# Optimization experiments

Measured on AMD Instinct MI355X. Metric: run time of the kernel, lower is better.

The kernel has to match this reference:

```python
import jax, jax.numpy as jnp
import numpy as np

S, B, H, E, V, T = 160, 64, 1024, 512, 64, 16


def setup_inputs() -> dict:
    key = jax.random.key(0)
    ks = jax.random.split(key, 13)
    g = lambda k, shape, scale: jax.random.normal(k, shape, jnp.float32) * scale
    return dict(
        encoder_h0=g(ks[0], (1, B, H), 1.0),
        encoder_c0=g(ks[1], (1, B, H), 1.0),
        encoder_outputs=g(ks[2], (S, B, H), 1.0),
        encoder_lens=jax.random.randint(ks[3], (B,), 1, S + 1),
        tok_embed=g(ks[4], (1, E), 0.02),
        embed=g(ks[5], (V, E), 0.02),
        W_ih=g(ks[6], (4 * H, E), 1.0 / np.sqrt(E)),
        W_hh=g(ks[7], (4 * H, H), 1.0 / np.sqrt(H)),
        b_ih=jnp.zeros((4 * H,), jnp.float32),
        b_hh=jnp.zeros((4 * H,), jnp.float32),
        out_W=g(ks[8], (V, 2 * H), 1.0 / np.sqrt(2 * H)),
        out_b=jnp.zeros((V,), jnp.float32),
        enc_W=g(ks[9], (H, H), 1.0 / np.sqrt(H)),
        enc_b=jnp.zeros((H,), jnp.float32),
        dec_W=g(ks[10], (H, H), 1.0 / np.sqrt(H)),
        dec_b=jnp.zeros((H,), jnp.float32),
        attn_W=g(ks[11], (1, H), 1.0 / np.sqrt(H)),
        attn_b=jnp.zeros((1,), jnp.float32),
    )


def reference(encoder_h0, encoder_c0, encoder_outputs, encoder_lens,
              tok_embed, embed, W_ih, W_hh, b_ih, b_hh,
              out_W, out_b, enc_W, enc_b, dec_W, dec_b, attn_W, attn_b):
    S_, B_, H_ = encoder_outputs.shape
    h0, c0 = encoder_h0[0], encoder_c0[0]          # [B,H]; source re-feeds encoder_hidden each step
    invalid = jnp.arange(S_)[None, :] >= encoder_lens[:, None]   # [B,S] True where masked
    NEG = jnp.float32(-1e9)

    def step(embed_tok, _):
        # LSTM cell, torch gate order (i, f, g, o)
        gates = embed_tok @ W_ih.T + b_ih + h0 @ W_hh.T + b_hh   # [B,4H]
        i, f, g, o = jnp.split(gates, 4, axis=-1)
        c = jax.nn.sigmoid(f) * c0 + jax.nn.sigmoid(i) * jnp.tanh(g)
        out = jax.nn.sigmoid(o) * jnp.tanh(c)                    # [B,H]
        # additive (Bahdanau) attention scores
        enc_t = jnp.einsum('sbh,kh->sbk', encoder_outputs, enc_W) + enc_b   # [S,B,H]
        dec_t = out @ dec_W.T + dec_b                                       # [B,H]
        scores = (jnp.tanh(enc_t + dec_t[None]) @ attn_W[0] + attn_b[0]).T # [B,S]
        attn = jax.nn.softmax(jnp.where(invalid, NEG, scores), axis=-1)    # [B,S]
        context = jnp.einsum('bs,sbh->bh', attn, encoder_outputs)          # [B,H]
        combined = jnp.concatenate([context, out], axis=-1)                # [B,2H]
        probs = jax.nn.softmax(combined @ out_W.T + out_b, axis=-1)
        probs = probs / jnp.sum(probs, axis=-1, keepdims=True)             # source renormalizes
        tok = jnp.argmax(probs, axis=-1)                                   # greedy decode
        onehot = jax.nn.one_hot(tok, probs.shape[-1], dtype=probs.dtype)
        neg_ent = jnp.sum(jax.lax.stop_gradient(probs) * jnp.log(probs + 1e-6), axis=-1)
        logp = jnp.log(jnp.sum(probs * onehot, axis=-1) + 1e-6)
        return embed[tok], (tok, attn, neg_ent, logp)

    start = jnp.broadcast_to(tok_embed[0], (B_, tok_embed.shape[1]))  # <SOS> embedding
    _, (toks, attns, negents, logps) = jax.lax.scan(step, start, None, length=T)
    predicted_tokens = toks                            # [T,B]
    context_total = jnp.transpose(attns, (1, 0, 2))    # [B,T,S] (attention maps, as in source)
    return predicted_tokens, context_total, jnp.sum(negents, axis=0), jnp.sum(logps, axis=0)
```

## Files before the change

### kernel.cpp

```cpp
#include <hip/hip_runtime.h>

#define S_ 160
#define B_ 64
#define H_ 1024
#define E_ 512
#define V_ 64
#define T_ 16
#define H4_ 4096

__device__ __forceinline__ float sigm(float x) { return 1.f / (1.f + expf(-x)); }

__global__ __launch_bounds__(256) void gemm_bt_128(
    const float* __restrict__ A, const float* __restrict__ Bm,
    const float* __restrict__ bias, float* __restrict__ Cd,
    int M, int N, int K)
{
    __shared__ float As[16][132];
    __shared__ float Bs[16][132];
    const int bn = blockIdx.x, bm = blockIdx.y;
    const int tid = threadIdx.x;
    const int lr = tid >> 1, lk = (tid & 1) * 8;
    const int tx4 = (tid & 15) * 4, ty4 = (tid >> 4) * 4;
    const float* Ap = A + (size_t)(bm * 128 + lr) * K + lk;
    const float* Bp = Bm + (size_t)(bn * 128 + lr) * K + lk;
    float acc[8][8] = {};
    for (int k0 = 0; k0 < K; k0 += 16) {
        float4 a0 = *(const float4*)(Ap + k0);
        float4 a1 = *(const float4*)(Ap + k0 + 4);
        float4 b0 = *(const float4*)(Bp + k0);
        float4 b1 = *(const float4*)(Bp + k0 + 4);
        __syncthreads();
        As[lk + 0][lr] = a0.x; As[lk + 1][lr] = a0.y; As[lk + 2][lr] = a0.z; As[lk + 3][lr] = a0.w;
        As[lk + 4][lr] = a1.x; As[lk + 5][lr] = a1.y; As[lk + 6][lr] = a1.z; As[lk + 7][lr] = a1.w;
        Bs[lk + 0][lr] = b0.x; Bs[lk + 1][lr] = b0.y; Bs[lk + 2][lr] = b0.z; Bs[lk + 3][lr] = b0.w;
        Bs[lk + 4][lr] = b1.x; Bs[lk + 5][lr] = b1.y; Bs[lk + 6][lr] = b1.z; Bs[lk + 7][lr] = b1.w;
        __syncthreads();
#pragma unroll
        for (int kk = 0; kk < 16; ++kk) {
            float a[8], b[8];
            *(float4*)(a)     = *(const float4*)&As[kk][ty4];
            *(float4*)(a + 4) = *(const float4*)&As[kk][64 + ty4];
            *(float4*)(b)     = *(const float4*)&Bs[kk][tx4];
            *(float4*)(b + 4) = *(const float4*)&Bs[kk][64 + tx4];
#pragma unroll
            for (int i = 0; i < 8; ++i)
#pragma unroll
                for (int j = 0; j < 8; ++j) acc[i][j] = fmaf(a[i], b[j], acc[i][j]);
        }
    }
#pragma unroll
    for (int i = 0; i < 8; ++i) {
        int row = bm * 128 + ((i < 4) ? (ty4 + i) : (64 + ty4 + i - 4));
#pragma unroll
        for (int j = 0; j < 8; ++j) {
            int col = bn * 128 + ((j < 4) ? (tx4 + j) : (64 + tx4 + j - 4));
            Cd[(size_t)row * N + col] = acc[i][j] + bias[col];
        }
    }
}

__device__ __forceinline__ void tile64(const float* __restrict__ Arow,
                                       const float* __restrict__ Brow,
                                       int K, float acc[4][4],
                                       float* __restrict__ As,
                                       float* __restrict__ Bs)
{
    const int tid = threadIdx.x;
    const int lr = tid >> 2, lc = (tid & 3) << 2;
    const int tx = tid & 15, ty = tid >> 4;
    for (int k0 = 0; k0 < K; k0 += 16) {
        float4 av = *(const float4*)(Arow + k0);
        float4 bv = *(const float4*)(Brow + k0);
        __syncthreads();
        As[lr * 17 + lc + 0] = av.x; As[lr * 17 + lc + 1] = av.y;
        As[lr * 17 + lc + 2] = av.z; As[lr * 17 + lc + 3] = av.w;
        Bs[lr * 17 + lc + 0] = bv.x; Bs[lr * 17 + lc + 1] = bv.y;
        Bs[lr * 17 + lc + 2] = bv.z; Bs[lr * 17 + lc + 3] = bv.w;
        __syncthreads();
#pragma unroll
        for (int kk = 0; kk < 16; ++kk) {
            float a[4], b[4];
#pragma unroll
            for (int i = 0; i < 4; ++i) a[i] = As[(ty * 4 + i) * 17 + kk];
#pragma unroll
            for (int j = 0; j < 4; ++j) b[j] = Bs[(tx * 4 + j) * 17 + kk];
#pragma unroll
            for (int i = 0; i < 4; ++i)
#pragma unroll
                for (int j = 0; j < 4; ++j) acc[i][j] = fmaf(a[i], b[j], acc[i][j]);
        }
    }
    __syncthreads();
}

__global__ __launch_bounds__(256) void gemm_part(
    const float* __restrict__ A, const float* __restrict__ Bm,
    float* __restrict__ Cpart, int M, int N, int K)
{
    __shared__ float smem[2176];
    const int bn = blockIdx.x, bm = blockIdx.y, kz = blockIdx.z, KS = gridDim.z;
    const int tid = threadIdx.x;
    const int lr = tid >> 2, lc = (tid & 3) << 2;
    const int tx = tid & 15, ty = tid >> 4;
    const int kLen = K / KS, k0base = kz * kLen;
    float acc[4][4] = {};
    tile64(A + (size_t)(bm * 64 + lr) * K + k0base + lc,
           Bm + (size_t)(bn * 64 + lr) * K + k0base + lc,
           kLen, acc, smem, smem + 1088);
    float* Cp = Cpart + (size_t)kz * M * N;
#pragma unroll
    for (int i = 0; i < 4; ++i) {
        int row = bm * 64 + ty * 4 + i;
#pragma unroll
        for (int j = 0; j < 4; ++j)
            Cp[(size_t)row * N + bn * 64 + tx * 4 + j] = acc[i][j];
    }
}

__global__ void reduce_partials(const float* __restrict__ Cpart, int KS,
                                const float* __restrict__ bias,
                                const float* __restrict__ bias2,
                                float* __restrict__ C, int MN, int N)
{
    int idx = blockIdx.x * 256 + threadIdx.x;
    if (idx >= MN) return;
    float v = 0.f;
    for (int z = 0; z < KS; ++z) v += Cpart[(size_t)z * MN + idx];
    int col = idx % N;
    if (bias)  v += bias[col];
    if (bias2) v += bias2[col];
    C[idx] = v;
}

__global__ void init_k(const float* __restrict__ embed, const float* __restrict__ tok_emb,
                       float* __restrict__ emb_ext,
                       float* __restrict__ negent, float* __restrict__ logp)
{
    int i = blockIdx.x * 256 + threadIdx.x;
    if (i < 128 * E_) {
        int r = i >> 9, c = i & (E_ - 1);
        emb_ext[i] = (r < 64) ? embed[r * E_ + c] : ((r == 64) ? tok_emb[c] : 0.f);
    }
    if (i < B_) { negent[i] = 0.f; logp[i] = 0.f; }
}

__global__ __launch_bounds__(256) void lstm_gather_k(
    const float* __restrict__ all_gates, const float* __restrict__ gates_sel,
    const float* __restrict__ hh_gates, const float* __restrict__ enc_c0,
    float* __restrict__ out_h, int t)
{
    int idx = blockIdx.x * 256 + threadIdx.x;
    int b = idx >> 10, h = idx & (H_ - 1);
    const float* ag = (t == 0) ? (all_gates + (size_t)64 * H4_)
                               : (gates_sel + (size_t)b * H4_);
    const float* hg = hh_gates + (size_t)b * H4_;
    float gi = ag[h]           + hg[h];
    float gf = ag[H_ + h]      + hg[H_ + h];
    float gg = ag[2 * H_ + h]  + hg[2 * H_ + h];
    float go = ag[3 * H_ + h]  + hg[3 * H_ + h];
    float cc = sigm(gf) * enc_c0[idx] + sigm(gi) * tanhf(gg);
    out_h[idx] = sigm(go) * tanhf(cc);
}

__global__ __launch_bounds__(256) void score_k(
    const float* __restrict__ enc_t, const float* __restrict__ dec_part,
    const float* __restrict__ dec_b, const float* __restrict__ attn_W,
    const float* __restrict__ attn_b, const int* __restrict__ lens,
    float* __restrict__ scores)
{
    const int lane = threadIdx.x & 63;
    const int gw = blockIdx.x * 4 + (threadIdx.x >> 6);
    const int b = gw >> 5, sg = gw & 31;
    float dec_r[16], aw_r[16];
#pragma unroll
    for (int it = 0; it < 16; ++it) {
        int h = lane + it * 64;
        dec_r[it] = dec_part[(size_t)b * H_ + h]
                  + dec_part[(size_t)(B_ + b) * H_ + h]
                  + dec_part[(size_t)(2 * B_ + b) * H_ + h]
                  + dec_part[(size_t)(3 * B_ + b) * H_ + h]
                  + dec_b[h];
        aw_r[it] = attn_W[h];
    }
    const int len = lens[b];
    const float ab = attn_b[0];
    for (int s = sg * 5; s < sg * 5 + 5; ++s) {
        if (s >= len) { if (lane == 0) scores[b * S_ + s] = -1e9f; continue; }
        const float* ep = enc_t + ((size_t)s * B_ + b) * H_;
        float acc = 0.f;
#pragma unroll
        for (int it = 0; it < 16; ++it)
            acc += aw_r[it] * tanhf(ep[lane + it * 64] + dec_r[it]);
        for (int d = 32; d; d >>= 1) acc += __shfl_xor(acc, d);
        if (lane == 0) scores[b * S_ + s] = acc + ab;
    }
}

__global__ __launch_bounds__(256) void smax_out_k(
    const float* __restrict__ scores, const float* __restrict__ enc_out,
    const float* __restrict__ out_h, const float* __restrict__ out_W,
    const float* __restrict__ out_b, const float* __restrict__ all_gates,
    float* __restrict__ gates_sel,
    float* __restrict__ negent_acc, float* __restrict__ logp_acc,
    float* __restrict__ out, int t)
{
    __shared__ float sc[S_];
    __shared__ float comb[2 * H_];
    __shared__ float lg[V_];
    __shared__ int tok_s;
    const int tid = threadIdx.x;
    const int b = blockIdx.x;
    const int lane = tid & 63, wv = tid >> 6;
    if (wv == 0) {
        float m = -1e30f;
        for (int s = lane; s < S_; s += 64) {
            float v = scores[b * S_ + s]; sc[s] = v; m = fmaxf(m, v);
        }
        for (int d = 32; d; d >>= 1) m = fmaxf(m, __shfl_xor(m, d));
        float sum = 0.f;
        for (int s = lane; s < S_; s += 64) {
            float e = expf(sc[s] - m); sc[s] = e; sum += e;
        }
        for (int d = 32; d; d >>= 1) sum += __shfl_xor(sum, d);
        float inv = 1.f / sum;
        for (int s = lane; s < S_; s += 64) {
            float pr = sc[s] * inv; sc[s] = pr;
            out[T_ * B_ + ((size_t)b * T_ + t) * S_ + s] = pr;
        }
    }
    __syncthreads();
    {
        const float* base = enc_out + (size_t)b * H_ + tid * 4;
        float4 ac0 = {0,0,0,0}, ac1 = {0,0,0,0}, ac2 = {0,0,0,0}, ac3 = {0,0,0,0};
#pragma unroll 4
        for (int s = 0; s < S_; s += 4) {
            float4 e0 = *(const float4*)(base + (size_t)(s    ) * B_ * H_);
            float4 e1 = *(const float4*)(base + (size_t)(s + 1) * B_ * H_);
            float4 e2 = *(const float4*)(base + (size_t)(s + 2) * B_ * H_);
            float4 e3 = *(const float4*)(base + (size_t)(s + 3) * B_ * H_);
            float p0 = sc[s], p1 = sc[s + 1], p2 = sc[s + 2], p3 = sc[s + 3];
            ac0.x = fmaf(p0, e0.x, ac0.x); ac0.y = fmaf(p0, e0.y, ac0.y);
            ac0.z = fmaf(p0, e0.z, ac0.z); ac0.w = fmaf(p0, e0.w, ac0.w);
            ac1.x = fmaf(p1, e1.x, ac1.x); ac1.y = fmaf(p1, e1.y, ac1.y);
            ac1.z = fmaf(p1, e1.z, ac1.z); ac1.w = fmaf(p1, e1.w, ac1.w);
            ac2.x = fmaf(p2, e2.x, ac2.x); ac2.y = fmaf(p2, e2.y, ac2.y);
            ac2.z = fmaf(p2, e2.z, ac2.z); ac2.w = fmaf(p2, e2.w, ac2.w);
            ac3.x = fmaf(p3, e3.x, ac3.x); ac3.y = fmaf(p3, e3.y, ac3.y);
            ac3.z = fmaf(p3, e3.z, ac3.z); ac3.w = fmaf(p3, e3.w, ac3.w);
        }
        comb[tid * 4 + 0] = ac0.x + ac1.x + ac2.x + ac3.x;
        comb[tid * 4 + 1] = ac0.y + ac1.y + ac2.y + ac3.y;
        comb[tid * 4 + 2] = ac0.z + ac1.z + ac2.z + ac3.z;
        comb[tid * 4 + 3] = ac0.w + ac1.w + ac2.w + ac3.w;
    }
    for (int i = tid; i < H_; i += 256) comb[H_ + i] = out_h[(size_t)b * H_ + i];
    __syncthreads();
    for (int v = wv * 16; v < wv * 16 + 16; ++v) {
        const float* w = out_W + (size_t)v * (2 * H_);
        float a0 = 0.f, a1 = 0.f;
#pragma unroll
        for (int j = 0; j < 32; j += 2) {
            a0 = fmaf(comb[lane + j * 64], w[lane + j * 64], a0);
            a1 = fmaf(comb[lane + (j + 1) * 64], w[lane + (j + 1) * 64], a1);
        }
        float acc = a0 + a1;
        for (int d = 32; d; d >>= 1) acc += __shfl_xor(acc, d);
        if (lane == 0) lg[v] = acc + out_b[v];
    }
    __syncthreads();
    if (wv == 0) {
        float x = lg[lane];
        float m = x;
        for (int d = 32; d; d >>= 1) m = fmaxf(m, __shfl_xor(m, d));
        float e = expf(x - m);
        float s = e;
        for (int d = 32; d; d >>= 1) s += __shfl_xor(s, d);
        float pr = e / s;
        float ps = pr;
        for (int d = 32; d; d >>= 1) ps += __shfl_xor(ps, d);
        pr = pr / ps;
        float bv = pr; int bi = lane;
        for (int d = 32; d; d >>= 1) {
            float ov = __shfl_xor(bv, d); int oi = __shfl_xor(bi, d);
            if (ov > bv || (ov == bv && oi < bi)) { bv = ov; bi = oi; }
        }
        float ne = pr * logf(pr + 1e-6f);
        for (int d = 32; d; d >>= 1) ne += __shfl_xor(ne, d);
        float ptok = __shfl(pr, bi);
        if (lane == 0) {
            out[t * B_ + b] = (float)bi;
            float na = negent_acc[b] + ne;                negent_acc[b] = na;
            float la = logp_acc[b] + logf(ptok + 1e-6f);  logp_acc[b] = la;
            if (t == T_ - 1) {
                out[T_ * B_ + B_ * T_ * S_ + b] = na;
                out[T_ * B_ + B_ * T_ * S_ + B_ + b] = la;
            }
            tok_s = bi;
        }
    }
    __syncthreads();
    {
        const int tk = tok_s;
        const float4* src = (const float4*)(all_gates + (size_t)tk * H4_);
        float4* dst = (float4*)(gates_sel + (size_t)b * H4_);
        for (int i = tid; i < H4_ / 4; i += 256) dst[i] = src[i];
    }
}

extern "C" void kernel_launch(void* const* d_in, const int* in_sizes, int n_in,
                              void* d_out, int out_size, void* d_ws, size_t ws_size,
                              hipStream_t stream) {
    const float* enc_h0  = (const float*)d_in[0];
    const float* enc_c0  = (const float*)d_in[1];
    const float* enc_out = (const float*)d_in[2];
    const int*   lens    = (const int*)d_in[3];
    const float* tok_emb = (const float*)d_in[4];
    const float* embed   = (const float*)d_in[5];
    const float* W_ih    = (const float*)d_in[6];
    const float* W_hh    = (const float*)d_in[7];
    const float* b_ih    = (const float*)d_in[8];
    const float* b_hh    = (const float*)d_in[9];
    const float* out_W   = (const float*)d_in[10];
    const float* out_b   = (const float*)d_in[11];
    const float* enc_W   = (const float*)d_in[12];
    const float* enc_b   = (const float*)d_in[13];
    const float* dec_W   = (const float*)d_in[14];
    const float* dec_b   = (const float*)d_in[15];
    const float* attn_W  = (const float*)d_in[16];
    const float* attn_b  = (const float*)d_in[17];
    float* out = (float*)d_out;

    float* ws = (float*)d_ws;
    float* hh_gates  = ws;
    float* out_h     = hh_gates + B_ * H4_;
    float* dec_part  = out_h + B_ * H_;
    float* scores    = dec_part + 4 * B_ * H_;
    float* negent    = scores + B_ * S_;
    float* logp      = negent + B_;
    float* gates_sel = logp + B_;
    float* emb_ext   = gates_sel + B_ * H4_;
    float* all_gates = emb_ext + 128 * E_;
    float* enc_t     = all_gates + (size_t)128 * H4_;
    float* part      = enc_t;
    if (ws_size < 47751680u) return;

    init_k<<<(128 * E_ + 255) / 256, 256, 0, stream>>>(embed, tok_emb, emb_ext,
                                                       negent, logp);

    gemm_part<<<dim3(H4_ / 64, 1, 4), 256, 0, stream>>>(enc_h0, W_hh, part, B_, H4_, H_);
    reduce_partials<<<(B_ * H4_ + 255) / 256, 256, 0, stream>>>(
        part, 4, b_ih, b_hh, hh_gates, B_ * H4_, H4_);

    gemm_part<<<dim3(H4_ / 64, 2, 1), 256, 0, stream>>>(emb_ext, W_ih, all_gates,
                                                        128, H4_, E_);

    gemm_bt_128<<<dim3(H_ / 128, (S_ * B_) / 128), 256, 0, stream>>>(
        enc_out, enc_W, enc_b, enc_t, S_ * B_, H_, H_);

    for (int t = 0; t < T_; ++t) {
        lstm_gather_k<<<(B_ * H_) / 256, 256, 0, stream>>>(all_gates, gates_sel, hh_gates,
                                                           enc_c0, out_h, t);
        gemm_part<<<dim3(H_ / 64, 1, 4), 256, 0, stream>>>(out_h, dec_W, dec_part, B_, H_, H_);
        score_k<<<512, 256, 0, stream>>>(enc_t, dec_part, dec_b, attn_W, attn_b, lens, scores);
        smax_out_k<<<64, 256, 0, stream>>>(scores, enc_out, out_h, out_W, out_b,
                                           all_gates, gates_sel, negent, logp, out, t);
    }
}
```

Measured before the change: 1.629 ms.

## Retile enc GEMM to 512 threads, skip masked context rows, simplify gate source

```diff
diff --git a/kernel.cpp b/kernel.cpp
--- a/kernel.cpp
+++ b/kernel.cpp
@@ -10,7 +10,7 @@
 
 __device__ __forceinline__ float sigm(float x) { return 1.f / (1.f + expf(-x)); }
 
-__global__ __launch_bounds__(256) void gemm_bt_128(
+__global__ __launch_bounds__(512) void gemm_bt_128(
     const float* __restrict__ A, const float* __restrict__ Bm,
     const float* __restrict__ bias, float* __restrict__ Cd,
     int M, int N, int K)
@@ -19,41 +19,38 @@
     __shared__ float Bs[16][132];
     const int bn = blockIdx.x, bm = blockIdx.y;
     const int tid = threadIdx.x;
-    const int lr = tid >> 1, lk = (tid & 1) * 8;
-    const int tx4 = (tid & 15) * 4, ty4 = (tid >> 4) * 4;
+    const int lr = tid >> 2, lk = (tid & 3) * 4;
+    const int cx4 = (tid & 15) * 4, ry4 = (tid >> 4) * 4;
     const float* Ap = A + (size_t)(bm * 128 + lr) * K + lk;
     const float* Bp = Bm + (size_t)(bn * 128 + lr) * K + lk;
-    float acc[8][8] = {};
+    float acc[4][8] = {};
     for (int k0 = 0; k0 < K; k0 += 16) {
-        float4 a0 = *(const float4*)(Ap + k0);
-        float4 a1 = *(const float4*)(Ap + k0 + 4);
-        float4 b0 = *(const float4*)(Bp + k0);
-        float4 b1 = *(const float4*)(Bp + k0 + 4);
+        float4 av = *(const float4*)(Ap + k0);
+        float4 bv = *(const float4*)(Bp + k0);
         __syncthreads();
-        As[lk + 0][lr] = a0.x; As[lk + 1][lr] = a0.y; As[lk + 2][lr] = a0.z; As[lk + 3][lr] = a0.w;
-        As[lk + 4][lr] = a1.x; As[lk + 5][lr] = a1.y; As[lk + 6][lr] = a1.z; As[lk + 7][lr] = a1.w;
-        Bs[lk + 0][lr] = b0.x; Bs[lk + 1][lr] = b0.y; Bs[lk + 2][lr] = b0.z; Bs[lk + 3][lr] = b0.w;
-        Bs[lk + 4][lr] = b1.x; Bs[lk + 5][lr] = b1.y; Bs[lk + 6][lr] = b1.z; Bs[lk + 7][lr] = b1.w;
+        As[lk + 0][lr] = av.x; As[lk + 1][lr] = av.y;
+        As[lk + 2][lr] = av.z; As[lk + 3][lr] = av.w;
+        Bs[lk + 0][lr] = bv.x; Bs[lk + 1][lr] = bv.y;
+        Bs[lk + 2][lr] = bv.z; Bs[lk + 3][lr] = bv.w;
         __syncthreads();
 #pragma unroll
         for (int kk = 0; kk < 16; ++kk) {
-            float a[8], b[8];
-            *(float4*)(a)     = *(const float4*)&As[kk][ty4];
-            *(float4*)(a + 4) = *(const float4*)&As[kk][64 + ty4];
-            *(float4*)(b)     = *(const float4*)&Bs[kk][tx4];
-            *(float4*)(b + 4) = *(const float4*)&Bs[kk][64 + tx4];
-#pragma unroll
-            for (int i = 0; i < 8; ++i)
+            float a[4], b[8];
+            *(float4*)(a)     = *(const float4*)&As[kk][ry4];
+            *(float4*)(b)     = *(const float4*)&Bs[kk][cx4];
+            *(float4*)(b + 4) = *(const float4*)&Bs[kk][64 + cx4];
+#pragma unroll
+            for (int i = 0; i < 4; ++i)
 #pragma unroll
                 for (int j = 0; j < 8; ++j) acc[i][j] = fmaf(a[i], b[j], acc[i][j]);
         }
     }
 #pragma unroll
-    for (int i = 0; i < 8; ++i) {
-        int row = bm * 128 + ((i < 4) ? (ty4 + i) : (64 + ty4 + i - 4));
+    for (int i = 0; i < 4; ++i) {
+        int row = bm * 128 + ry4 + i;
 #pragma unroll
         for (int j = 0; j < 8; ++j) {
-            int col = bn * 128 + ((j < 4) ? (tx4 + j) : (64 + tx4 + j - 4));
+            int col = bn * 128 + ((j < 4) ? (cx4 + j) : (64 + cx4 + j - 4));
             Cd[(size_t)row * N + col] = acc[i][j] + bias[col];
         }
     }
@@ -145,14 +142,13 @@
 }
 
 __global__ __launch_bounds__(256) void lstm_gather_k(
-    const float* __restrict__ all_gates, const float* __restrict__ gates_sel,
+    const float* __restrict__ gsrc, size_t strideB,
     const float* __restrict__ hh_gates, const float* __restrict__ enc_c0,
-    float* __restrict__ out_h, int t)
+    float* __restrict__ out_h)
 {
     int idx = blockIdx.x * 256 + threadIdx.x;
     int b = idx >> 10, h = idx & (H_ - 1);
-    const float* ag = (t == 0) ? (all_gates + (size_t)64 * H4_)
-                               : (gates_sel + (size_t)b * H4_);
+    const float* ag = gsrc + (size_t)b * strideB;
     const float* hg = hh_gates + (size_t)b * H4_;
     float gi = ag[h]           + hg[h];
     float gf = ag[H_ + h]      + hg[H_ + h];
@@ -200,7 +196,7 @@
     const float* __restrict__ scores, const float* __restrict__ enc_out,
     const float* __restrict__ out_h, const float* __restrict__ out_W,
     const float* __restrict__ out_b, const float* __restrict__ all_gates,
-    float* __restrict__ gates_sel,
+    const int* __restrict__ lens, float* __restrict__ gates_sel,
     float* __restrict__ negent_acc, float* __restrict__ logp_acc,
     float* __restrict__ out, int t)
 {
@@ -230,10 +226,10 @@
     }
     __syncthreads();
     {
+        const int len4 = (lens[b] + 3) & ~3;
         const float* base = enc_out + (size_t)b * H_ + tid * 4;
         float4 ac0 = {0,0,0,0}, ac1 = {0,0,0,0}, ac2 = {0,0,0,0}, ac3 = {0,0,0,0};
-#pragma unroll 4
-        for (int s = 0; s < S_; s += 4) {
+        for (int s = 0; s < len4; s += 4) {
             float4 e0 = *(const float4*)(base + (size_t)(s    ) * B_ * H_);
             float4 e1 = *(const float4*)(base + (size_t)(s + 1) * B_ * H_);
             float4 e2 = *(const float4*)(base + (size_t)(s + 2) * B_ * H_);
@@ -354,15 +350,17 @@
     gemm_part<<<dim3(H4_ / 64, 2, 1), 256, 0, stream>>>(emb_ext, W_ih, all_gates,
                                                         128, H4_, E_);
 
-    gemm_bt_128<<<dim3(H_ / 128, (S_ * B_) / 128), 256, 0, stream>>>(
+    gemm_bt_128<<<dim3(H_ / 128, (S_ * B_) / 128), 512, 0, stream>>>(
         enc_out, enc_W, enc_b, enc_t, S_ * B_, H_, H_);
 
     for (int t = 0; t < T_; ++t) {
-        lstm_gather_k<<<(B_ * H_) / 256, 256, 0, stream>>>(all_gates, gates_sel, hh_gates,
-                                                           enc_c0, out_h, t);
+        const float* gsrc = (t == 0) ? (all_gates + (size_t)64 * H4_) : gates_sel;
+        const size_t strideB = (t == 0) ? 0 : (size_t)H4_;
+        lstm_gather_k<<<(B_ * H_) / 256, 256, 0, stream>>>(gsrc, strideB, hh_gates,
+                                                           enc_c0, out_h);
         gemm_part<<<dim3(H_ / 64, 1, 4), 256, 0, stream>>>(out_h, dec_W, dec_part, B_, H_, H_);
         score_k<<<512, 256, 0, stream>>>(enc_t, dec_part, dec_b, attn_W, attn_b, lens, scores);
         smax_out_k<<<64, 256, 0, stream>>>(scores, enc_out, out_h, out_W, out_b,
-                                           all_gates, gates_sel, negent, logp, out, t);
-    }
-}
+                                           all_gates, lens, gates_sel, negent, logp, out, t);
+    }
+}
```

Measured after the change: 1.663 ms. 2.1% more time.
